# Kernel tuning notes

Measured on AMD Instinct MI355X. Metric: run time of the kernel, lower is better.

## Reference

```python
import jax, jax.numpy as jnp
import numpy as np

B, D, H, K = 8192, 1280, 16384, 64


def setup_inputs() -> dict:
    key = jax.random.key(0)
    k1, k2, k3 = jax.random.split(key, 3)
    x = jax.random.normal(k1, (B, D), dtype=jnp.float32)
    # encoder weight [hidden_dim, input_dim] (torch Linear layout)
    W_enc = jax.random.normal(k2, (H, D), dtype=jnp.float32) * (1.0 / np.sqrt(D))
    b_enc = jnp.zeros((H,), dtype=jnp.float32)
    # decoder weight [input_dim, hidden_dim], unit-norm columns scaled by 0.1
    W_dec = jax.random.normal(k3, (D, H), dtype=jnp.float32)
    W_dec = 0.1 * W_dec / jnp.linalg.norm(W_dec, axis=0, keepdims=True)
    b_dec = jnp.zeros((D,), dtype=jnp.float32)
    b_pre = jnp.zeros((D,), dtype=jnp.float32)
    return {"x": x, "W_enc": W_enc, "b_enc": b_enc, "W_dec": W_dec,
            "b_dec": b_dec, "b_pre": b_pre, "k": K}


def reference(x, W_enc, b_enc, W_dec, b_dec, b_pre, k):
    # --- encode ---
    x_centered = x - b_pre                                   # [B, D]
    pre = jnp.einsum('bd,hd->bh', x_centered, W_enc) + b_enc  # [B, H]
    vals, idx = jax.lax.top_k(pre, k)                        # [B, k]
    rows = jnp.arange(pre.shape[0])[:, None]                 # [B, 1]
    hidden = jnp.zeros_like(pre).at[rows, idx].set(jax.nn.relu(vals))  # [B, H]
    # --- decode ---
    reconstructed = jnp.einsum('bh,dh->bd', hidden, W_dec) + b_dec + b_pre
    # --- losses ---
    reconstruction_loss = jnp.mean((reconstructed - x) ** 2)
    l0 = jnp.mean(jnp.sum((hidden > 0).astype(jnp.float32), axis=-1))
    sparsity_loss = jnp.array(0.0, dtype=jnp.float32)
    loss = reconstruction_loss
    return reconstructed, hidden, loss, reconstruction_loss, sparsity_loss, l0
```

## Files before the change

### kernel.cpp

```cpp
#include <hip/hip_runtime.h>
#include <hip/hip_bf16.h>

constexpr int K_MAX    = 128;
constexpr int S_MAX    = 128;
constexpr int A_MAX    = 256;
constexpr int CAND_MAX = 512;
constexpr int BM = 128, BN = 128, BKF = 16;
constexpr int NBITER = 42;
constexpr int D_MAX   = 2048;
constexpr int H_FIX   = 16384;

typedef __attribute__((ext_vector_type(8))) short bf16x8;
typedef __attribute__((ext_vector_type(8))) unsigned short u16x8;
typedef __attribute__((ext_vector_type(4))) float f32x4;

__device__ inline unsigned short f2bf(float f) {
  unsigned u = __float_as_uint(f);
  return (unsigned short)((u + 0x7fff + ((u >> 16) & 1)) >> 16);
}
__device__ inline unsigned short key_of(float f) {
  unsigned short b = f2bf(f);
  return b ^ ((b & 0x8000) ? 0xFFFF : 0x8000);
}
__device__ inline float val_of_key(unsigned short kk) {
  unsigned short b = (kk & 0x8000) ? (unsigned short)(kk ^ 0x8000)
                                   : (unsigned short)(kk ^ 0xFFFF);
  return __uint_as_float(((unsigned)b) << 16);
}
__device__ inline float bf2f(unsigned short b) {
  return __uint_as_float(((unsigned)b) << 16);
}

__device__ inline int lds_slot(int r, int c) {
  return ((r >> 1) << 4) | ((r & 1) << 3) | (c ^ ((r >> 1) & 7));
}

__global__ __launch_bounds__(256) void prep_xb(
    const float* __restrict__ x, const float* __restrict__ b_pre,
    unsigned short* __restrict__ Xb, int D, size_t total4)
{
  for (size_t i = blockIdx.x * 256 + threadIdx.x; i < total4; i += (size_t)gridDim.x * 256) {
    const size_t e = i * 4;
    const int d = (int)(e % D);
    float4 xv = *reinterpret_cast<const float4*>(x + e);
    float4 bp = *reinterpret_cast<const float4*>(b_pre + d);
    ushort4 o;
    o.x = f2bf(xv.x - bp.x); o.y = f2bf(xv.y - bp.y);
    o.z = f2bf(xv.z - bp.z); o.w = f2bf(xv.w - bp.w);
    *reinterpret_cast<ushort4*>(Xb + e) = o;
  }
}

__global__ __launch_bounds__(256) void prep_wb(
    const float* __restrict__ W, unsigned short* __restrict__ Wb, size_t total4)
{
  for (size_t i = blockIdx.x * 256 + threadIdx.x; i < total4; i += (size_t)gridDim.x * 256) {
    const size_t e = i * 4;
    float4 wv = *reinterpret_cast<const float4*>(W + e);
    ushort4 o;
    o.x = f2bf(wv.x); o.y = f2bf(wv.y); o.z = f2bf(wv.z); o.w = f2bf(wv.w);
    *reinterpret_cast<ushort4*>(Wb + e) = o;
  }
}

__global__ __launch_bounds__(256) void enc_gemm_bf16(
    const unsigned short* __restrict__ Xb, const unsigned short* __restrict__ Wb,
    const float* __restrict__ b_enc, float* __restrict__ pre, int D, int H)
{
  __shared__ unsigned short As[2][128 * 64];
  __shared__ unsigned short Bs[2][128 * 64];
  const int tid  = threadIdx.x;
  const int wave = tid >> 6, lane = tid & 63;
  const int m0 = blockIdx.y * 128, n0 = blockIdx.x * 128;
  const int wm = (wave >> 1) * 64, wn = (wave & 1) * 64;
  const int l16 = lane & 15, lhi = lane >> 4;

  f32x4 acc[4][4];
#pragma unroll
  for (int i = 0; i < 4; ++i)
#pragma unroll
    for (int j = 0; j < 4; ++j) acc[i][j] = (f32x4){0.f, 0.f, 0.f, 0.f};

  const int NT = D / 64;

#pragma unroll
  for (int i = 0; i < 4; ++i) {
    const int base = wave * 64 + i * 256;
    const int idx  = base + lane;
    const int sr = idx >> 4, u = idx & 15;
    const int row = (sr << 1) | (u >> 3);
    const int ch  = (u & 7) ^ (sr & 7);
    __builtin_amdgcn_global_load_lds(
        (const __attribute__((address_space(1))) unsigned int*)(Xb + (size_t)(m0 + row) * D + ch * 8),
        (__attribute__((address_space(3))) unsigned int*)(As[0] + (size_t)base * 8), 16, 0, 0);
    __builtin_amdgcn_global_load_lds(
        (const __attribute__((address_space(1))) unsigned int*)(Wb + (size_t)(n0 + row) * D + ch * 8),
        (__attribute__((address_space(3))) unsigned int*)(Bs[0] + (size_t)base * 8), 16, 0, 0);
  }
  __syncthreads();

  int cur = 0;
  for (int t = 0; t < NT; ++t) {
    if (t + 1 < NT) {
      const int kb = (t + 1) * 64;
      const int nxt = cur ^ 1;
#pragma unroll
      for (int i = 0; i < 4; ++i) {
        const int base = wave * 64 + i * 256;
        const int idx  = base + lane;
        const int sr = idx >> 4, u = idx & 15;
        const int row = (sr << 1) | (u >> 3);
        const int ch  = (u & 7) ^ (sr & 7);
        __builtin_amdgcn_global_load_lds(
            (const __attribute__((address_space(1))) unsigned int*)(Xb + (size_t)(m0 + row) * D + kb + ch * 8),
            (__attribute__((address_space(3))) unsigned int*)(As[nxt] + (size_t)base * 8), 16, 0, 0);
        __builtin_amdgcn_global_load_lds(
            (const __attribute__((address_space(1))) unsigned int*)(Wb + (size_t)(n0 + row) * D + kb + ch * 8),
            (__attribute__((address_space(3))) unsigned int*)(Bs[nxt] + (size_t)base * 8), 16, 0, 0);
      }
    }
#pragma unroll
    for (int kk = 0; kk < 2; ++kk) {
      bf16x8 af[4], bfr[4];
#pragma unroll
      for (int mi = 0; mi < 4; ++mi)
        af[mi] = *reinterpret_cast<const bf16x8*>(
            As[cur] + (size_t)lds_slot(wm + mi * 16 + l16, kk * 4 + lhi) * 8);
#pragma unroll
      for (int ni = 0; ni < 4; ++ni)
        bfr[ni] = *reinterpret_cast<const bf16x8*>(
            Bs[cur] + (size_t)lds_slot(wn + ni * 16 + l16, kk * 4 + lhi) * 8);
#pragma unroll
      for (int mi = 0; mi < 4; ++mi)
#pragma unroll
        for (int ni = 0; ni < 4; ++ni)
          acc[mi][ni] = __builtin_amdgcn_mfma_f32_16x16x32_bf16(af[mi], bfr[ni], acc[mi][ni], 0, 0, 0);
    }
    __syncthreads();
    cur ^= 1;
  }

#pragma unroll
  for (int ni = 0; ni < 4; ++ni) {
    const int n = n0 + wn + ni * 16 + l16;
    const float be = b_enc[n];
#pragma unroll
    for (int mi = 0; mi < 4; ++mi) {
      const int mbase = m0 + wm + mi * 16 + lhi * 4;
#pragma unroll
      for (int r = 0; r < 4; ++r) {
        unsigned short* prow = (unsigned short*)(pre + (size_t)(mbase + r) * H);
        prow[n] = key_of(acc[mi][ni][r] + be);
      }
    }
  }
}

__global__ __launch_bounds__(256) void topk_classify_keys(
    float* __restrict__ hidden,
    int* __restrict__ sure_ix, float* __restrict__ sure_val, int* __restrict__ sure_cnt,
    int* __restrict__ amb_ix, int* __restrict__ amb_cnt,
    const int* __restrict__ kptr, float delta)
{
  constexpr int H = H_FIX, NC = H_FIX / (256 * 8);
  __shared__ int hist[4096];
  __shared__ int chunk[256];
  __shared__ int misc[8];

  const int tid = threadIdx.x, b = blockIdx.x;
  const int k = min(*kptr, K_MAX);
  float* hrow = hidden + (size_t)b * H;
  const unsigned short* krow = (const unsigned short*)hrow;

  if (tid < 8) misc[tid] = 0;
  for (int i = tid; i < 4096; i += 256) hist[i] = 0;

  u16x8 kv[NC];
#pragma unroll
  for (int i = 0; i < NC; ++i)
    kv[i] = *reinterpret_cast<const u16x8*>(krow + ((size_t)i * 256 + tid) * 8);
  __syncthreads();

  const float4 z4 = {0.f, 0.f, 0.f, 0.f};
  for (int i = tid; i < (H >> 2); i += 256)
    reinterpret_cast<float4*>(hrow)[i] = z4;

#pragma unroll
  for (int i = 0; i < NC; ++i)
#pragma unroll
    for (int j = 0; j < 8; ++j)
      atomicAdd(&hist[((unsigned)(unsigned short)kv[i][j]) >> 4], 1);
  __syncthreads();

  int csum = 0;
#pragma unroll
  for (int j = 0; j < 16; ++j) csum += hist[tid * 16 + j];
  chunk[tid] = csum;
  __syncthreads();
  int gt = 0;
  for (int j = tid + 1; j < 256; ++j) gt += chunk[j];
  {
    int run = gt;
#pragma unroll
    for (int j = 15; j >= 0; --j) {
      const int hc = hist[tid * 16 + j];
      if (run < k && k <= run + hc) { misc[0] = tid * 16 + j; misc[1] = run; }
      run += hc;
    }
  }
  __syncthreads();
  const int b1 = misc[0];
  if (tid < 16) chunk[tid] = 0;
  __syncthreads();
#pragma unroll
  for (int i = 0; i < NC; ++i)
#pragma unroll
    for (int j = 0; j < 8; ++j) {
      const unsigned kk = (unsigned)(unsigned short)kv[i][j];
      if ((int)(kk >> 4) == b1) atomicAdd(&chunk[kk & 15], 1);
    }
  __syncthreads();
  if (tid == 0) {
    int run = misc[1];
    int K16 = b1 << 4;
    for (int j = 15; j >= 0; --j) {
      const int c = chunk[j];
      if (run < k && k <= run + c) K16 = (b1 << 4) | j;
      run += c;
    }
    const float v_lo = val_of_key((unsigned short)K16);
    const float v_hi = val_of_key((unsigned short)min(K16 + 1, 65535));
    const float ulp = v_hi - v_lo;
    const float vs = v_hi + delta;
    const float va = v_lo - ulp - delta;
    int ks = key_of(vs); if (val_of_key((unsigned short)ks) > vs) --ks;
    int ka = key_of(va); if (val_of_key((unsigned short)ka) < va) ++ka;
    misc[2] = ks; misc[3] = ka;
  }
  __syncthreads();
  const unsigned ks = (unsigned)misc[2], ka = (unsigned)misc[3];

#pragma unroll
  for (int i = 0; i < NC; ++i)
#pragma unroll
    for (int j = 0; j < 8; ++j) {
      const unsigned kk = (unsigned)(unsigned short)kv[i][j];
      if (kk > ks) {
        const int p = atomicAdd(&misc[4], 1);
        if (p < S_MAX) {
          const int h = (i * 256 + tid) * 8 + j;
          sure_ix[(size_t)b * S_MAX + p] = h;
          sure_val[(size_t)b * S_MAX + p] = val_of_key((unsigned short)kk);
        }
      } else if (kk >= ka) {
        const int p = atomicAdd(&misc[5], 1);
        if (p < A_MAX) amb_ix[(size_t)b * A_MAX + p] = (i * 256 + tid) * 8 + j;
      }
    }
  __syncthreads();
  if (tid == 0) {
    sure_cnt[b] = min(misc[4], S_MAX);
    amb_cnt[b]  = min(misc[5], A_MAX);
  }
}

__global__ __launch_bounds__(256) void refine_scatter(
    const float* __restrict__ X, const float* __restrict__ b_pre,
    const float* __restrict__ W, const float* __restrict__ b_enc,
    const int* __restrict__ sure_ix, const float* __restrict__ sure_val,
    const int* __restrict__ sure_cnt,
    const int* __restrict__ amb_ix, const int* __restrict__ amb_cnt,
    const int* __restrict__ kptr,
    float* __restrict__ hidden, int* __restrict__ tk_idx, float* __restrict__ tk_val, int D)
{
  constexpr int H = H_FIX;
  __shared__ float  xr[D_MAX];
  __shared__ double asv[A_MAX];
  __shared__ int    aix[A_MAX];
  const int tid = threadIdx.x, b = blockIdx.x;
  const int k = min(*kptr, K_MAX);
  const int S = min(min(sure_cnt[b], S_MAX), k);
  const int A = min(amb_cnt[b], A_MAX);
  float* hrow = hidden + (size_t)b * H;

  for (int d = tid; d < D; d += 256) xr[d] = X[(size_t)b * D + d] - b_pre[d];
  for (int c = tid; c < A; c += 256) aix[c] = amb_ix[(size_t)b * A_MAX + c];

  for (int i = tid; i < S; i += 256) {
    const int h = sure_ix[(size_t)b * S_MAX + i];
    const float v = sure_val[(size_t)b * S_MAX + i];
    const float rv = (v > 0.f) ? v : 0.f;
    hrow[h] = rv;
    tk_idx[(size_t)b * K_MAX + i] = h;
    tk_val[(size_t)b * K_MAX + i] = rv;
  }
  __syncthreads();

  const int wid = tid >> 6, lane = tid & 63;
  for (int c = wid; c < A; c += 4) {
    const int h = aix[c];
    const float* wr = W + (size_t)h * D;
    double s0 = 0.0, s1 = 0.0;
    int i = lane;
    for (; i + 64 < D; i += 128) {
      s0 += (double)xr[i] * (double)wr[i];
      s1 += (double)xr[i + 64] * (double)wr[i + 64];
    }
    if (i < D) s0 += (double)xr[i] * (double)wr[i];
    double s = s0 + s1;
    for (int off = 32; off; off >>= 1) s += __shfl_xor(s, off);
    if (lane == 0) asv[c] = s + (double)b_enc[h];
  }
  __syncthreads();

  const int m = k - S;
  for (int c = tid; c < A; c += 256) {
    const double v = asv[c];
    const int h = aix[c];
    int r = 0;
    for (int j = 0; j < A; ++j) {
      const double vj = asv[j];
      r += ((vj > v) || (vj == v && aix[j] < h)) ? 1 : 0;
    }
    if (r < m) {
      const float rv = (v > 0.0) ? (float)v : 0.f;
      hrow[h] = rv;
      tk_idx[(size_t)b * K_MAX + S + r] = h;
      tk_val[(size_t)b * K_MAX + S + r] = rv;
    }
  }
}

__global__ __launch_bounds__(256, 2) void topk_select(
    const float* __restrict__ X, const float* __restrict__ b_pre,
    const float* __restrict__ W, const float* __restrict__ b_enc,
    float* __restrict__ hidden, int* __restrict__ tk_idx, float* __restrict__ tk_val,
    const int* __restrict__ kptr, int D, float margin)
{
  constexpr int H = H_FIX, NC = H_FIX / (256 * 8);
  __shared__ double cand_sv[CAND_MAX];
  __shared__ float  xr[D_MAX];
  __shared__ int    cand_ix[CAND_MAX];
  __shared__ int    hist[4096];
  __shared__ int    chunk[256];
  __shared__ int    misc[8];

  const int tid = threadIdx.x, b = blockIdx.x;
  const int k = min(*kptr, K_MAX);
  float* hrow = hidden + (size_t)b * H;
  const unsigned short* krow = (const unsigned short*)hrow;

  if (tid < 8) misc[tid] = 0;
  for (int i = tid; i < 4096; i += 256) hist[i] = 0;
  for (int d = tid; d < D; d += 256) xr[d] = X[(size_t)b * D + d] - b_pre[d];

  u16x8 kv[NC];
#pragma unroll
  for (int i = 0; i < NC; ++i)
    kv[i] = *reinterpret_cast<const u16x8*>(krow + ((size_t)i * 256 + tid) * 8);
  __syncthreads();

#pragma unroll
  for (int i = 0; i < NC; ++i)
#pragma unroll
    for (int j = 0; j < 8; ++j)
      atomicAdd(&hist[((unsigned)(unsigned short)kv[i][j]) >> 4], 1);
  __syncthreads();

  int csum = 0;
#pragma unroll
  for (int j = 0; j < 16; ++j) csum += hist[tid * 16 + j];
  chunk[tid] = csum;
  __syncthreads();
  int gt = 0;
  for (int j = tid + 1; j < 256; ++j) gt += chunk[j];
  {
    int run = gt;
#pragma unroll
    for (int j = 15; j >= 0; --j) {
      const int hc = hist[tid * 16 + j];
      if (run < k && k <= run + hc) { misc[0] = tid * 16 + j; misc[1] = run; }
      run += hc;
    }
  }
  __syncthreads();
  const int b1 = misc[0];
  if (tid < 16) chunk[tid] = 0;
  __syncthreads();
#pragma unroll
  for (int i = 0; i < NC; ++i)
#pragma unroll
    for (int j = 0; j < 8; ++j) {
      const unsigned kk = (unsigned)(unsigned short)kv[i][j];
      if ((int)(kk >> 4) == b1) atomicAdd(&chunk[kk & 15], 1);
    }
  __syncthreads();
  if (tid == 0) {
    int run = misc[1];
    int K16 = b1 << 4;
    for (int j = 15; j >= 0; --j) {
      const int c = chunk[j];
      if (run < k && k <= run + c) K16 = (b1 << 4) | j;
      run += c;
    }
    const float vthr = val_of_key((unsigned short)K16) - margin;
    int kt = (int)key_of(vthr);
    if (kt > K16) kt = K16;
    misc[2] = kt;
  }
  __syncthreads();
  const unsigned kthr = (unsigned)misc[2];

#pragma unroll
  for (int i = 0; i < NC; ++i)
#pragma unroll
    for (int j = 0; j < 8; ++j) {
      if ((unsigned)(unsigned short)kv[i][j] >= kthr) {
        const int pos = atomicAdd(&misc[3], 1);
        if (pos < CAND_MAX) cand_ix[pos] = (i * 256 + tid) * 8 + j;
      }
    }
  __syncthreads();
  const int C = min(misc[3], CAND_MAX);

  const float4 z4 = {0.f, 0.f, 0.f, 0.f};
  for (int i = tid; i < (H >> 2); i += 256)
    reinterpret_cast<float4*>(hrow)[i] = z4;

  const int wid = tid >> 6, lane = tid & 63;
  for (int c = wid; c < C; c += 4) {
    const int h = cand_ix[c];
    const float* wr = W + (size_t)h * D;
    double s = 0.0;
    for (int i = lane; i < D; i += 64) s += (double)xr[i] * (double)wr[i];
    for (int off = 32; off; off >>= 1) s += __shfl_xor(s, off);
    if (lane == 0) cand_sv[c] = s + (double)b_enc[h];
  }
  __syncthreads();

  for (int c = tid; c < C; c += 256) {
    const double v = cand_sv[c];
    const int h = cand_ix[c];
    int r = 0;
    for (int j = 0; j < C; ++j) {
      const double vj = cand_sv[j];
      r += ((vj > v) || (vj == v && cand_ix[j] < h)) ? 1 : 0;
    }
    if (r < k) {
      const float rv = (v > 0.0) ? (float)v : 0.f;
      hrow[h] = rv;
      tk_idx[(size_t)b * K_MAX + r] = h;
      tk_val[(size_t)b * K_MAX + r] = rv;
    }
  }
}

__global__ __launch_bounds__(256) void enc_gemm_f32(
    const float* __restrict__ X, const float* __restrict__ W,
    const float* __restrict__ b_enc, const float* __restrict__ b_pre,
    float* __restrict__ pre, int D, int H)
{
  __shared__ float As[BKF][BM + 4];
  __shared__ float Bs[BKF][BN + 4];
  const int tid = threadIdx.x;
  const int m0 = blockIdx.y * BM;
  const int n0 = blockIdx.x * BN;
  const int tx = tid & 15, ty = tid >> 4;
  float acc[8][8];
#pragma unroll
  for (int i = 0; i < 8; ++i)
#pragma unroll
    for (int j = 0; j < 8; ++j) acc[i][j] = 0.f;

  for (int kb = 0; kb < D; kb += BKF) {
#pragma unroll
    for (int t = 0; t < 2; ++t) {
      const int f4i = tid + t * 256;
      const int row = f4i >> 2;
      const int kq  = (f4i & 3) << 2;
      float4 xv = *reinterpret_cast<const float4*>(X + (size_t)(m0 + row) * D + kb + kq);
      float4 bp = *reinterpret_cast<const float4*>(b_pre + kb + kq);
      As[kq + 0][row] = xv.x - bp.x; As[kq + 1][row] = xv.y - bp.y;
      As[kq + 2][row] = xv.z - bp.z; As[kq + 3][row] = xv.w - bp.w;
      float4 wv = *reinterpret_cast<const float4*>(W + (size_t)(n0 + row) * D + kb + kq);
      Bs[kq + 0][row] = wv.x; Bs[kq + 1][row] = wv.y;
      Bs[kq + 2][row] = wv.z; Bs[kq + 3][row] = wv.w;
    }
    __syncthreads();
#pragma unroll
    for (int kk = 0; kk < BKF; ++kk) {
      float4 a0 = *reinterpret_cast<const float4*>(&As[kk][ty * 8]);
      float4 a1 = *reinterpret_cast<const float4*>(&As[kk][ty * 8 + 4]);
      float4 b0 = *reinterpret_cast<const float4*>(&Bs[kk][tx * 8]);
      float4 b1 = *reinterpret_cast<const float4*>(&Bs[kk][tx * 8 + 4]);
      float av[8] = {a0.x, a0.y, a0.z, a0.w, a1.x, a1.y, a1.z, a1.w};
      float bv[8] = {b0.x, b0.y, b0.z, b0.w, b1.x, b1.y, b1.z, b1.w};
#pragma unroll
      for (int i = 0; i < 8; ++i)
#pragma unroll
        for (int j = 0; j < 8; ++j) acc[i][j] += av[i] * bv[j];
    }
    __syncthreads();
  }
#pragma unroll
  for (int i = 0; i < 8; ++i) {
    const size_t m = (size_t)(m0 + ty * 8 + i);
#pragma unroll
    for (int j = 0; j < 8; j += 4) {
      const int n = n0 + tx * 8 + j;
      float4 o;
      o.x = acc[i][j + 0] + b_enc[n + 0];
      o.y = acc[i][j + 1] + b_enc[n + 1];
      o.z = acc[i][j + 2] + b_enc[n + 2];
      o.w = acc[i][j + 3] + b_enc[n + 3];
      *reinterpret_cast<float4*>(pre + m * H + n) = o;
    }
  }
}

__global__ __launch_bounds__(256) void topk_refine(
    const float* __restrict__ X, const float* __restrict__ b_pre,
    const float* __restrict__ W, const float* __restrict__ b_enc,
    float* __restrict__ hidden, int* __restrict__ tk_idx, float* __restrict__ tk_val,
    const int* __restrict__ kptr, int D, int H, float margin)
{
  extern __shared__ char smem_raw[];
  double* cand_val = reinterpret_cast<double*>(smem_raw);
  float*  xr       = reinterpret_cast<float*>(cand_val + CAND_MAX);
  int*    cand_idx = reinterpret_cast<int*>(xr + D);
  int*    misc     = cand_idx + CAND_MAX;

  const int tid = threadIdx.x;
  const int b = blockIdx.x;
  const int k = min(*kptr, K_MAX);
  float* hrow = hidden + (size_t)b * H;

  for (int i = tid; i < NBITER + 2; i += 256) misc[i] = 0;
  for (int d = tid; d < D; d += 256) xr[d] = X[(size_t)b * D + d] - b_pre[d];

  float f[64];
#pragma unroll
  for (int i = 0; i < 16; ++i) {
    const int base = i * 1024 + tid * 4;
    float4 v = {-3e38f, -3e38f, -3e38f, -3e38f};
    if (base + 3 < H) v = *reinterpret_cast<const float4*>(hrow + base);
    f[4 * i + 0] = v.x; f[4 * i + 1] = v.y; f[4 * i + 2] = v.z; f[4 * i + 3] = v.w;
  }
  __syncthreads();

  float lo = -1e4f, hi = 1e4f;
  for (int it = 0; it < NBITER; ++it) {
    const float mid = 0.5f * (lo + hi);
    int cnt = 0;
#pragma unroll
    for (int j = 0; j < 64; ++j) cnt += (f[j] >= mid) ? 1 : 0;
    for (int off = 32; off; off >>= 1) cnt += __shfl_xor(cnt, off);
    if ((tid & 63) == 0) atomicAdd(&misc[it], cnt);
    __syncthreads();
    if (misc[it] >= k) lo = mid; else hi = mid;
  }

  const float thresh = lo - margin;
#pragma unroll
  for (int j = 0; j < 64; ++j) {
    if (f[j] >= thresh) {
      const int h = (j >> 2) * 1024 + tid * 4 + (j & 3);
      if (h < H) {
        int pos = atomicAdd(&misc[NBITER], 1);
        if (pos < CAND_MAX) cand_idx[pos] = h;
      }
    }
  }
  __syncthreads();
  const int C = min(misc[NBITER], CAND_MAX);

  const int wid = tid >> 6, lane = tid & 63;
  for (int c = wid; c < C; c += 4) {
    const int h = cand_idx[c];
    const float* wr = W + (size_t)h * D;
    double s = 0.0;
    for (int i = lane; i < D; i += 64) s += (double)xr[i] * (double)wr[i];
    for (int off = 32; off; off >>= 1) s += __shfl_xor(s, off);
    if (lane == 0) cand_val[c] = s + (double)b_enc[h];
  }
  __syncthreads();

  const float4 z4 = {0.f, 0.f, 0.f, 0.f};
  for (int i = tid; i < (H >> 2); i += 256)
    reinterpret_cast<float4*>(hrow)[i] = z4;
  __syncthreads();

  for (int c = tid; c < C; c += 256) {
    const double v = cand_val[c];
    const int h = cand_idx[c];
    int r = 0;
    for (int j = 0; j < C; ++j) {
      const double vj = cand_val[j];
      r += ((vj > v) || (vj == v && cand_idx[j] < h)) ? 1 : 0;
    }
    if (r < k) {
      const float rv = (v > 0.0) ? (float)v : 0.f;
      hrow[h] = rv;
      tk_idx[(size_t)b * K_MAX + r] = h;
      tk_val[(size_t)b * K_MAX + r] = rv;
    }
  }
}

__global__ __launch_bounds__(256) void transpose_wdec_bf16(
    const float* __restrict__ Wsrc, unsigned short* __restrict__ WT, int D, int H)
{
  __shared__ float tile[32][33];
  const int c  = threadIdx.x & 31;
  const int r0 = threadIdx.x >> 5;
  const int h0 = blockIdx.x * 32;
  const int d0 = blockIdx.y * 32;
#pragma unroll
  for (int r = r0; r < 32; r += 8) {
    const int d = d0 + r, h = h0 + c;
    if (d < D && h < H) tile[r][c] = Wsrc[(size_t)d * H + h];
  }
  __syncthreads();
#pragma unroll
  for (int r = r0; r < 32; r += 8) {
    const int h = h0 + r, d = d0 + c;
    if (h < H && d < D) WT[(size_t)h * D + d] = f2bf(tile[c][r]);
  }
}

__global__ __launch_bounds__(256) void decode_loss(
    const float* __restrict__ X, const float* __restrict__ b_pre,
    const float* __restrict__ b_dec, const float* __restrict__ Wfull,
    const unsigned short* __restrict__ WTb,
    const int* __restrict__ tk_idx, const float* __restrict__ tk_val,
    const int* __restrict__ kptr,
    float* __restrict__ recon, double* __restrict__ row_ssq,
    int D, int H, int useWT)
{
  __shared__ int   sidx[K_MAX];
  __shared__ float sval[K_MAX];
  __shared__ double sd[4];
  const int tid = threadIdx.x, b = blockIdx.x;
  const int k = min(*kptr, K_MAX);
  if (tid < k) {
    sidx[tid] = tk_idx[(size_t)b * K_MAX + tid];
    sval[tid] = tk_val[(size_t)b * K_MAX + tid];
  }
  __syncthreads();
  double ssq = 0.0;
  const int D4 = D >> 2;
  for (int dc = tid; dc < D4; dc += 256) {
    const int d = dc * 4;
    float4 bd = *reinterpret_cast<const float4*>(b_dec + d);
    float4 bp = *reinterpret_cast<const float4*>(b_pre + d);
    float4 a = {bd.x + bp.x, bd.y + bp.y, bd.z + bp.z, bd.w + bp.w};
    if (useWT) {
#pragma unroll 4
      for (int j = 0; j < k; ++j) {
        const ushort4 w = *reinterpret_cast<const ushort4*>(WTb + (size_t)sidx[j] * D + d);
        const float s = sval[j];
        a.x += s * bf2f(w.x); a.y += s * bf2f(w.y);
        a.z += s * bf2f(w.z); a.w += s * bf2f(w.w);
      }
    } else {
#pragma unroll 4
      for (int j = 0; j < k; ++j) {
        const float s = sval[j];
        const int h = sidx[j];
        a.x += s * Wfull[(size_t)(d + 0) * H + h];
        a.y += s * Wfull[(size_t)(d + 1) * H + h];
        a.z += s * Wfull[(size_t)(d + 2) * H + h];
        a.w += s * Wfull[(size_t)(d + 3) * H + h];
      }
    }
    *reinterpret_cast<float4*>(recon + (size_t)b * D + d) = a;
    float4 xv = *reinterpret_cast<const float4*>(X + (size_t)b * D + d);
    const double d0 = (double)a.x - (double)xv.x;
    const double d1 = (double)a.y - (double)xv.y;
    const double d2 = (double)a.z - (double)xv.z;
    const double d3 = (double)a.w - (double)xv.w;
    ssq += d0 * d0 + d1 * d1 + d2 * d2 + d3 * d3;
  }
  for (int off = 32; off; off >>= 1) ssq += __shfl_xor(ssq, off);
  if ((tid & 63) == 0) sd[tid >> 6] = ssq;
  __syncthreads();
  if (tid == 0) row_ssq[b] = sd[0] + sd[1] + sd[2] + sd[3];
}

__global__ __launch_bounds__(256) void finalize_part(
    const double* __restrict__ row_ssq, const float* __restrict__ tk_val,
    const int* __restrict__ kptr, double* __restrict__ part_s, int* __restrict__ part_c,
    int Bdim, int rows_per_blk)
{
  __shared__ double sd[4];
  __shared__ int si[4];
  const int tid = threadIdx.x;
  const int k = min(*kptr, K_MAX);
  const int b0 = blockIdx.x * rows_per_blk;
  const int b1 = min(b0 + rows_per_blk, Bdim);
  double s = 0.0;
  for (int i = b0 + tid; i < b1; i += 256) s += row_ssq[i];
  int cnt = 0;
  const int total = (b1 - b0) * k;
  for (int i = tid; i < total; i += 256) {
    const int bb = b0 + i / k, j = i - (i / k) * k;
    cnt += (tk_val[(size_t)bb * K_MAX + j] > 0.f) ? 1 : 0;
  }
  for (int off = 32; off; off >>= 1) { s += __shfl_xor(s, off); cnt += __shfl_xor(cnt, off); }
  if ((tid & 63) == 0) { sd[tid >> 6] = s; si[tid >> 6] = cnt; }
  __syncthreads();
  if (tid == 0) {
    part_s[blockIdx.x] = sd[0] + sd[1] + sd[2] + sd[3];
    part_c[blockIdx.x] = si[0] + si[1] + si[2] + si[3];
  }
}

__global__ __launch_bounds__(64) void finalize_k2(
    const double* __restrict__ part_s, const int* __restrict__ part_c,
    float* __restrict__ scalars, int nparts, int Bdim, int D)
{
  const int tid = threadIdx.x;
  double s = (tid < nparts) ? part_s[tid] : 0.0;
  int cnt = (tid < nparts) ? part_c[tid] : 0;
  for (int off = 32; off; off >>= 1) { s += __shfl_xor(s, off); cnt += __shfl_xor(cnt, off); }
  if (tid == 0) {
    const double rl = s / ((double)Bdim * (double)D);
    scalars[0] = (float)rl;
    scalars[1] = (float)rl;
    scalars[2] = 0.f;
    scalars[3] = (float)((double)cnt / Bdim);
  }
}

extern "C" void kernel_launch(void* const* d_in, const int* in_sizes, int n_in,
                              void* d_out, int out_size, void* d_ws, size_t ws_size,
                              hipStream_t stream)
{
  const float* x     = (const float*)d_in[0];
  const float* W_enc = (const float*)d_in[1];
  const float* b_enc = (const float*)d_in[2];
  const float* W_dec = (const float*)d_in[3];
  const float* b_dec = (const float*)d_in[4];
  const float* b_pre = (const float*)d_in[5];
  const int*   kptr  = (const int*)d_in[6];

  const int D = in_sizes[4];
  const int H = in_sizes[2];
  const int B = in_sizes[0] / D;

  float* recon   = (float*)d_out;
  float* hidden  = recon + (size_t)B * D;
  float* scalars = hidden + (size_t)B * H;

  size_t off = 0;
  int* tk_idx = (int*)((char*)d_ws + off);        off += (size_t)B * K_MAX * sizeof(int);
  float* tk_val = (float*)((char*)d_ws + off);    off += (size_t)B * K_MAX * sizeof(float);
  off = (off + 7) & ~(size_t)7;
  double* row_ssq = (double*)((char*)d_ws + off); off += (size_t)B * sizeof(double);
  double* part_s = (double*)((char*)d_ws + off);  off += 64 * sizeof(double);
  int* part_c = (int*)((char*)d_ws + off);        off += 64 * sizeof(int);
  off = (off + 7) & ~(size_t)7;

  unsigned short* Xb = (unsigned short*)((char*)d_ws + off);
  off += (size_t)B * D * sizeof(unsigned short);
  unsigned short* Wb = (unsigned short*)((char*)d_ws + off);
  off += (size_t)H * D * sizeof(unsigned short);
  const int useBF16 = (off <= ws_size) ? 1 : 0;

  unsigned short* WTb = (unsigned short*)((char*)d_ws + off);
  off += (size_t)D * H * sizeof(unsigned short);
  const int useWT = (off <= ws_size) ? 1 : 0;

  int* sure_ix = (int*)((char*)d_ws + off);       off += (size_t)B * S_MAX * sizeof(int);
  float* sure_val = (float*)((char*)d_ws + off);  off += (size_t)B * S_MAX * sizeof(float);
  int* sure_cnt = (int*)((char*)d_ws + off);      off += (size_t)B * sizeof(int);
  int* amb_ix = (int*)((char*)d_ws + off);        off += (size_t)B * A_MAX * sizeof(int);
  int* amb_cnt = (int*)((char*)d_ws + off);       off += (size_t)B * sizeof(int);
  off = (off + 7) & ~(size_t)7;
  const int useSPLIT = (useBF16 && off <= ws_size) ? 1 : 0;

  const bool fast_ok = (D % 64 == 0) && (D <= D_MAX) &&
                       (H == H_FIX) && (B % 128 == 0);

  if (useBF16 && fast_ok) {
    const size_t tx4 = (size_t)B * D / 4, tw4 = (size_t)H * D / 4;
    prep_xb<<<2048, 256, 0, stream>>>(x, b_pre, Xb, D, tx4);
    prep_wb<<<2048, 256, 0, stream>>>(W_enc, Wb, tw4);
    dim3 gg(H / 128, B / 128);
    enc_gemm_bf16<<<gg, 256, 0, stream>>>(Xb, Wb, b_enc, hidden, D, H);
    if (useSPLIT) {
      topk_classify_keys<<<B, 256, 0, stream>>>(hidden, sure_ix, sure_val, sure_cnt,
                                                amb_ix, amb_cnt, kptr, 0.05f);
      refine_scatter<<<B, 256, 0, stream>>>(x, b_pre, W_enc, b_enc,
                                            sure_ix, sure_val, sure_cnt,
                                            amb_ix, amb_cnt, kptr,
                                            hidden, tk_idx, tk_val, D);
    } else {
      topk_select<<<B, 256, 0, stream>>>(x, b_pre, W_enc, b_enc, hidden,
                                         tk_idx, tk_val, kptr, D, 0.04f);
    }
  } else {
    dim3 gg(H / BN, B / BM);
    enc_gemm_f32<<<gg, 256, 0, stream>>>(x, W_enc, b_enc, b_pre, hidden, D, H);
    const size_t sh = CAND_MAX * sizeof(double) + (size_t)D * sizeof(float)
                    + CAND_MAX * sizeof(int) + (NBITER + 8) * sizeof(int);
    topk_refine<<<B, 256, sh, stream>>>(x, b_pre, W_enc, b_enc, hidden,
                                        tk_idx, tk_val, kptr, D, H, 1e-3f);
  }

  if (useWT)
    transpose_wdec_bf16<<<dim3((H + 31) / 32, (D + 31) / 32), 256, 0, stream>>>(W_dec, WTb, D, H);

  decode_loss<<<B, 256, 0, stream>>>(x, b_pre, b_dec, W_dec, WTb,
                                     tk_idx, tk_val, kptr, recon, row_ssq, D, H, useWT);

  const int rpb = (B + 63) / 64;
  finalize_part<<<64, 256, 0, stream>>>(row_ssq, tk_val, kptr, part_s, part_c, B, rpb);
  finalize_k2<<<1, 64, 0, stream>>>(part_s, part_c, scalars, 64, B, D);
}
```

Measured before the change: 1.136 ms.

## Enlarge encoder GEMM tile to 256x256 with interleaved staged loads

The bf16 encoder GEMM moves from a 128x128 tile with 256 threads to a 256x256 tile with 512 threads (8 waves, each computing 64x128). Global-to-LDS loads for the next k-step are split into quarters and interleaved with MFMA groups, using explicit vmcnt waits, raw barriers and s_setprio around the MFMA bursts. The goal is more arithmetic per LDS byte and better overlap of loads with compute. In exchange it uses 64KB of LDS per block and many more accumulator registers, which can cut occupancy. The unused topk_select fallback is removed.

```diff
diff --git a/kernel.cpp b/kernel.cpp
--- a/kernel.cpp
+++ b/kernel.cpp
@@ -63,85 +63,149 @@
   }
 }
 
-__global__ __launch_bounds__(256) void enc_gemm_bf16(
+__global__ __launch_bounds__(512, 2) void enc_gemm_bf16(
     const unsigned short* __restrict__ Xb, const unsigned short* __restrict__ Wb,
     const float* __restrict__ b_enc, float* __restrict__ pre, int D, int H)
 {
-  __shared__ unsigned short As[2][128 * 64];
-  __shared__ unsigned short Bs[2][128 * 64];
+  __shared__ unsigned short As[2][2048 * 8];
+  __shared__ unsigned short Bs[2][2048 * 8];
   const int tid  = threadIdx.x;
   const int wave = tid >> 6, lane = tid & 63;
-  const int m0 = blockIdx.y * 128, n0 = blockIdx.x * 128;
-  const int wm = (wave >> 1) * 64, wn = (wave & 1) * 64;
+  const int m0 = blockIdx.y * 256, n0 = blockIdx.x * 256;
+  const int wm = (wave >> 1) * 64;
+  const int wn = (wave & 1) * 128;
   const int l16 = lane & 15, lhi = lane >> 4;
 
-  f32x4 acc[4][4];
+  f32x4 acc[4][8];
 #pragma unroll
   for (int i = 0; i < 4; ++i)
 #pragma unroll
-    for (int j = 0; j < 4; ++j) acc[i][j] = (f32x4){0.f, 0.f, 0.f, 0.f};
+    for (int j = 0; j < 8; ++j) acc[i][j] = (f32x4){0.f, 0.f, 0.f, 0.f};
 
   const int NT = D / 64;
 
-#pragma unroll
-  for (int i = 0; i < 4; ++i) {
-    const int base = wave * 64 + i * 256;
-    const int idx  = base + lane;
-    const int sr = idx >> 4, u = idx & 15;
-    const int row = (sr << 1) | (u >> 3);
-    const int ch  = (u & 7) ^ (sr & 7);
+  auto stageA = [&](int buf, int h, int kb) {
+#pragma unroll
+    for (int i = 0; i < 2; ++i) {
+      const int idx = i * 512 + wave * 64 + lane;
+      const int sr = idx >> 4, u = idx & 15;
+      const int r  = (sr << 1) | (u >> 3);
+      const int ch = (u & 7) ^ (sr & 7);
+      __builtin_amdgcn_global_load_lds(
+          (const __attribute__((address_space(1))) unsigned int*)
+              (Xb + (size_t)(m0 + h * 128 + r) * D + kb + ch * 8),
+          (__attribute__((address_space(3))) unsigned int*)
+              (&As[buf][(size_t)(h * 1024 + idx) * 8]), 16, 0, 0);
+    }
+  };
+  auto stageBq = [&](int buf, int q, int kb) {
+    const int s  = (q & 1) * 512 + wave * 64 + lane;
+    const int sr = s >> 4, u = s & 15;
+    const int r  = (sr << 1) | (u >> 3);
+    const int ch = (u & 7) ^ (sr & 7);
     __builtin_amdgcn_global_load_lds(
-        (const __attribute__((address_space(1))) unsigned int*)(Xb + (size_t)(m0 + row) * D + ch * 8),
-        (__attribute__((address_space(3))) unsigned int*)(As[0] + (size_t)base * 8), 16, 0, 0);
-    __builtin_amdgcn_global_load_lds(
-        (const __attribute__((address_space(1))) unsigned int*)(Wb + (size_t)(n0 + row) * D + ch * 8),
-        (__attribute__((address_space(3))) unsigned int*)(Bs[0] + (size_t)base * 8), 16, 0, 0);
-  }
-  __syncthreads();
+        (const __attribute__((address_space(1))) unsigned int*)
+            (Wb + (size_t)(n0 + (q >> 1) * 128 + r) * D + kb + ch * 8),
+        (__attribute__((address_space(3))) unsigned int*)
+            (&Bs[buf][(size_t)((q >> 1) * 1024 + s) * 8]), 16, 0, 0);
+  };
+  auto readA = [&](int buf, int mi, int kk) -> bf16x8 {
+    const int gr = wm + mi * 16 + l16;
+    return *reinterpret_cast<const bf16x8*>(
+        &As[buf][(size_t)((gr >> 7) * 1024 + lds_slot(gr & 127, kk * 4 + lhi)) * 8]);
+  };
+  auto readB = [&](int buf, int ni, int kk) -> bf16x8 {
+    const int gr = wn + ni * 16 + l16;
+    return *reinterpret_cast<const bf16x8*>(
+        &Bs[buf][(size_t)((gr >> 7) * 1024 + lds_slot(gr & 127, kk * 4 + lhi)) * 8]);
+  };
+
+  stageA(0, 0, 0); stageA(0, 1, 0);
+  stageBq(0, 0, 0); stageBq(0, 2, 0);
+  stageBq(0, 1, 0); stageBq(0, 3, 0);
 
   int cur = 0;
   for (int t = 0; t < NT; ++t) {
-    if (t + 1 < NT) {
-      const int kb = (t + 1) * 64;
-      const int nxt = cur ^ 1;
-#pragma unroll
-      for (int i = 0; i < 4; ++i) {
-        const int base = wave * 64 + i * 256;
-        const int idx  = base + lane;
-        const int sr = idx >> 4, u = idx & 15;
-        const int row = (sr << 1) | (u >> 3);
-        const int ch  = (u & 7) ^ (sr & 7);
-        __builtin_amdgcn_global_load_lds(
-            (const __attribute__((address_space(1))) unsigned int*)(Xb + (size_t)(m0 + row) * D + kb + ch * 8),
-            (__attribute__((address_space(3))) unsigned int*)(As[nxt] + (size_t)base * 8), 16, 0, 0);
-        __builtin_amdgcn_global_load_lds(
-            (const __attribute__((address_space(1))) unsigned int*)(Wb + (size_t)(n0 + row) * D + kb + ch * 8),
-            (__attribute__((address_space(3))) unsigned int*)(Bs[nxt] + (size_t)base * 8), 16, 0, 0);
-      }
-    }
-#pragma unroll
-    for (int kk = 0; kk < 2; ++kk) {
-      bf16x8 af[4], bfr[4];
-#pragma unroll
-      for (int mi = 0; mi < 4; ++mi)
-        af[mi] = *reinterpret_cast<const bf16x8*>(
-            As[cur] + (size_t)lds_slot(wm + mi * 16 + l16, kk * 4 + lhi) * 8);
-#pragma unroll
-      for (int ni = 0; ni < 4; ++ni)
-        bfr[ni] = *reinterpret_cast<const bf16x8*>(
-            Bs[cur] + (size_t)lds_slot(wn + ni * 16 + l16, kk * 4 + lhi) * 8);
-#pragma unroll
-      for (int mi = 0; mi < 4; ++mi)
-#pragma unroll
-        for (int ni = 0; ni < 4; ++ni)
-          acc[mi][ni] = __builtin_amdgcn_mfma_f32_16x16x32_bf16(af[mi], bfr[ni], acc[mi][ni], 0, 0, 0);
-    }
-    __syncthreads();
-    cur ^= 1;
-  }
-
-#pragma unroll
-  for (int ni = 0; ni < 4; ++ni) {
+    const int nxt = cur ^ 1;
+    const int kb1 = (t + 1) * 64;
+    const bool more = (t + 1 < NT);
+
+    bf16x8 af[4][2], bf[2][2];
+
+    asm volatile("s_waitcnt vmcnt(2)" ::: "memory");
+    __builtin_amdgcn_s_barrier();
+#pragma unroll
+    for (int mi = 0; mi < 4; ++mi)
+#pragma unroll
+      for (int kk = 0; kk < 2; ++kk) af[mi][kk] = readA(cur, mi, kk);
+#pragma unroll
+    for (int j = 0; j < 2; ++j)
+#pragma unroll
+      for (int kk = 0; kk < 2; ++kk) bf[j][kk] = readB(cur, j, kk);
+    if (more) stageA(nxt, 0, kb1);
+    __builtin_amdgcn_s_setprio(1);
+#pragma unroll
+    for (int mi = 0; mi < 4; ++mi)
+#pragma unroll
+      for (int j = 0; j < 2; ++j)
+#pragma unroll
+        for (int kk = 0; kk < 2; ++kk)
+          acc[mi][j] = __builtin_amdgcn_mfma_f32_16x16x32_bf16(af[mi][kk], bf[j][kk], acc[mi][j], 0, 0, 0);
+    __builtin_amdgcn_s_setprio(0);
+
+#pragma unroll
+    for (int j = 0; j < 2; ++j)
+#pragma unroll
+      for (int kk = 0; kk < 2; ++kk) bf[j][kk] = readB(cur, 2 + j, kk);
+    if (more) stageA(nxt, 1, kb1);
+    __builtin_amdgcn_s_setprio(1);
+#pragma unroll
+    for (int mi = 0; mi < 4; ++mi)
+#pragma unroll
+      for (int j = 0; j < 2; ++j)
+#pragma unroll
+        for (int kk = 0; kk < 2; ++kk)
+          acc[mi][2 + j] = __builtin_amdgcn_mfma_f32_16x16x32_bf16(af[mi][kk], bf[j][kk], acc[mi][2 + j], 0, 0, 0);
+    __builtin_amdgcn_s_setprio(0);
+
+    if (more) { asm volatile("s_waitcnt vmcnt(4)" ::: "memory"); }
+    else      { asm volatile("s_waitcnt vmcnt(0)" ::: "memory"); }
+    __builtin_amdgcn_s_barrier();
+#pragma unroll
+    for (int j = 0; j < 2; ++j)
+#pragma unroll
+      for (int kk = 0; kk < 2; ++kk) bf[j][kk] = readB(cur, 4 + j, kk);
+    if (more) { stageBq(nxt, 0, kb1); stageBq(nxt, 2, kb1); }
+    __builtin_amdgcn_s_setprio(1);
+#pragma unroll
+    for (int mi = 0; mi < 4; ++mi)
+#pragma unroll
+      for (int j = 0; j < 2; ++j)
+#pragma unroll
+        for (int kk = 0; kk < 2; ++kk)
+          acc[mi][4 + j] = __builtin_amdgcn_mfma_f32_16x16x32_bf16(af[mi][kk], bf[j][kk], acc[mi][4 + j], 0, 0, 0);
+    __builtin_amdgcn_s_setprio(0);
+
+#pragma unroll
+    for (int j = 0; j < 2; ++j)
+#pragma unroll
+      for (int kk = 0; kk < 2; ++kk) bf[j][kk] = readB(cur, 6 + j, kk);
+    if (more) { stageBq(nxt, 1, kb1); stageBq(nxt, 3, kb1); }
+    __builtin_amdgcn_s_setprio(1);
+#pragma unroll
+    for (int mi = 0; mi < 4; ++mi)
+#pragma unroll
+      for (int j = 0; j < 2; ++j)
+#pragma unroll
+        for (int kk = 0; kk < 2; ++kk)
+          acc[mi][6 + j] = __builtin_amdgcn_mfma_f32_16x16x32_bf16(af[mi][kk], bf[j][kk], acc[mi][6 + j], 0, 0, 0);
+    __builtin_amdgcn_s_setprio(0);
+
+    cur = nxt;
+  }
+
+#pragma unroll
+  for (int ni = 0; ni < 8; ++ni) {
     const int n = n0 + wn + ni * 16 + l16;
     const float be = b_enc[n];
 #pragma unroll
@@ -327,130 +391,6 @@
       hrow[h] = rv;
       tk_idx[(size_t)b * K_MAX + S + r] = h;
       tk_val[(size_t)b * K_MAX + S + r] = rv;
-    }
-  }
-}
-
-__global__ __launch_bounds__(256, 2) void topk_select(
-    const float* __restrict__ X, const float* __restrict__ b_pre,
-    const float* __restrict__ W, const float* __restrict__ b_enc,
-    float* __restrict__ hidden, int* __restrict__ tk_idx, float* __restrict__ tk_val,
-    const int* __restrict__ kptr, int D, float margin)
-{
-  constexpr int H = H_FIX, NC = H_FIX / (256 * 8);
-  __shared__ double cand_sv[CAND_MAX];
-  __shared__ float  xr[D_MAX];
-  __shared__ int    cand_ix[CAND_MAX];
-  __shared__ int    hist[4096];
-  __shared__ int    chunk[256];
-  __shared__ int    misc[8];
-
-  const int tid = threadIdx.x, b = blockIdx.x;
-  const int k = min(*kptr, K_MAX);
-  float* hrow = hidden + (size_t)b * H;
-  const unsigned short* krow = (const unsigned short*)hrow;
-
-  if (tid < 8) misc[tid] = 0;
-  for (int i = tid; i < 4096; i += 256) hist[i] = 0;
-  for (int d = tid; d < D; d += 256) xr[d] = X[(size_t)b * D + d] - b_pre[d];
-
-  u16x8 kv[NC];
-#pragma unroll
-  for (int i = 0; i < NC; ++i)
-    kv[i] = *reinterpret_cast<const u16x8*>(krow + ((size_t)i * 256 + tid) * 8);
-  __syncthreads();
-
-#pragma unroll
-  for (int i = 0; i < NC; ++i)
-#pragma unroll
-    for (int j = 0; j < 8; ++j)
-      atomicAdd(&hist[((unsigned)(unsigned short)kv[i][j]) >> 4], 1);
-  __syncthreads();
-
-  int csum = 0;
-#pragma unroll
-  for (int j = 0; j < 16; ++j) csum += hist[tid * 16 + j];
-  chunk[tid] = csum;
-  __syncthreads();
-  int gt = 0;
-  for (int j = tid + 1; j < 256; ++j) gt += chunk[j];
-  {
-    int run = gt;
-#pragma unroll
-    for (int j = 15; j >= 0; --j) {
-      const int hc = hist[tid * 16 + j];
-      if (run < k && k <= run + hc) { misc[0] = tid * 16 + j; misc[1] = run; }
-      run += hc;
-    }
-  }
-  __syncthreads();
-  const int b1 = misc[0];
-  if (tid < 16) chunk[tid] = 0;
-  __syncthreads();
-#pragma unroll
-  for (int i = 0; i < NC; ++i)
-#pragma unroll
-    for (int j = 0; j < 8; ++j) {
-      const unsigned kk = (unsigned)(unsigned short)kv[i][j];
-      if ((int)(kk >> 4) == b1) atomicAdd(&chunk[kk & 15], 1);
-    }
-  __syncthreads();
-  if (tid == 0) {
-    int run = misc[1];
-    int K16 = b1 << 4;
-    for (int j = 15; j >= 0; --j) {
-      const int c = chunk[j];
-      if (run < k && k <= run + c) K16 = (b1 << 4) | j;
-      run += c;
-    }
-    const float vthr = val_of_key((unsigned short)K16) - margin;
-    int kt = (int)key_of(vthr);
-    if (kt > K16) kt = K16;
-    misc[2] = kt;
-  }
-  __syncthreads();
-  const unsigned kthr = (unsigned)misc[2];
-
-#pragma unroll
-  for (int i = 0; i < NC; ++i)
-#pragma unroll
-    for (int j = 0; j < 8; ++j) {
-      if ((unsigned)(unsigned short)kv[i][j] >= kthr) {
-        const int pos = atomicAdd(&misc[3], 1);
-        if (pos < CAND_MAX) cand_ix[pos] = (i * 256 + tid) * 8 + j;
-      }
-    }
-  __syncthreads();
-  const int C = min(misc[3], CAND_MAX);
-
-  const float4 z4 = {0.f, 0.f, 0.f, 0.f};
-  for (int i = tid; i < (H >> 2); i += 256)
-    reinterpret_cast<float4*>(hrow)[i] = z4;
-
-  const int wid = tid >> 6, lane = tid & 63;
-  for (int c = wid; c < C; c += 4) {
-    const int h = cand_ix[c];
-    const float* wr = W + (size_t)h * D;
-    double s = 0.0;
-    for (int i = lane; i < D; i += 64) s += (double)xr[i] * (double)wr[i];
-    for (int off = 32; off; off >>= 1) s += __shfl_xor(s, off);
-    if (lane == 0) cand_sv[c] = s + (double)b_enc[h];
-  }
-  __syncthreads();
-
-  for (int c = tid; c < C; c += 256) {
-    const double v = cand_sv[c];
-    const int h = cand_ix[c];
-    int r = 0;
-    for (int j = 0; j < C; ++j) {
-      const double vj = cand_sv[j];
-      r += ((vj > v) || (vj == v && cand_ix[j] < h)) ? 1 : 0;
-    }
-    if (r < k) {
-      const float rv = (v > 0.0) ? (float)v : 0.f;
-      hrow[h] = rv;
-      tk_idx[(size_t)b * K_MAX + r] = h;
-      tk_val[(size_t)b * K_MAX + r] = rv;
     }
   }
 }
@@ -780,25 +720,20 @@
   const int useSPLIT = (useBF16 && off <= ws_size) ? 1 : 0;
 
   const bool fast_ok = (D % 64 == 0) && (D <= D_MAX) &&
-                       (H == H_FIX) && (B % 128 == 0);
-
-  if (useBF16 && fast_ok) {
+                       (H == H_FIX) && (B % 256 == 0);
+
+  if (useBF16 && fast_ok && useSPLIT) {
     const size_t tx4 = (size_t)B * D / 4, tw4 = (size_t)H * D / 4;
     prep_xb<<<2048, 256, 0, stream>>>(x, b_pre, Xb, D, tx4);
     prep_wb<<<2048, 256, 0, stream>>>(W_enc, Wb, tw4);
-    dim3 gg(H / 128, B / 128);
-    enc_gemm_bf16<<<gg, 256, 0, stream>>>(Xb, Wb, b_enc, hidden, D, H);
-    if (useSPLIT) {
-      topk_classify_keys<<<B, 256, 0, stream>>>(hidden, sure_ix, sure_val, sure_cnt,
-                                                amb_ix, amb_cnt, kptr, 0.05f);
-      refine_scatter<<<B, 256, 0, stream>>>(x, b_pre, W_enc, b_enc,
-                                            sure_ix, sure_val, sure_cnt,
-                                            amb_ix, amb_cnt, kptr,
-                                            hidden, tk_idx, tk_val, D);
-    } else {
-      topk_select<<<B, 256, 0, stream>>>(x, b_pre, W_enc, b_enc, hidden,
-                                         tk_idx, tk_val, kptr, D, 0.04f);
-    }
+    dim3 gg(H / 256, B / 256);
+    enc_gemm_bf16<<<gg, 512, 0, stream>>>(Xb, Wb, b_enc, hidden, D, H);
+    topk_classify_keys<<<B, 256, 0, stream>>>(hidden, sure_ix, sure_val, sure_cnt,
+                                              amb_ix, amb_cnt, kptr, 0.05f);
+    refine_scatter<<<B, 256, 0, stream>>>(x, b_pre, W_enc, b_enc,
+                                          sure_ix, sure_val, sure_cnt,
+                                          amb_ix, amb_cnt, kptr,
+                                          hidden, tk_idx, tk_val, D);
   } else {
     dim3 gg(H / BN, B / BM);
     enc_gemm_f32<<<gg, 256, 0, stream>>>(x, W_enc, b_enc, b_pre, hidden, D, H);
```

Result: faster. 994.5 us (-12.5%).
